# Kernel optimization log

Measured on AMD Instinct MI355X. Metric: run time of the kernel, lower is better.

Reference implementation:

```python
import math
import jax, jax.numpy as jnp
import numpy as np

B, T, M, D = 65536, 20, 4, 4   # batch, timesteps, regions, d_reg
L, H, FF = 3, 2, 16            # layers, heads, dim_feedforward
S = M + 1                      # seq_len with cls token
TAU = 10000.0


def setup_inputs() -> dict:
    key = jax.random.key(0)
    ks = jax.random.split(key, 8)

    def w(k, shape, std=0.1):
        return jax.random.normal(k, shape, dtype=jnp.float32) * std

    return {
        "regional_states": jax.random.normal(ks[0], (B, T, M, D), dtype=jnp.float32),
        "cls_token": w(ks[1], (1, 1, D), 0.02),
        # stacked per-layer params (layer axis first)
        "Wqkv": w(ks[2], (L, 3 * D, D)),   # nn.MultiheadAttention in_proj_weight
        "bqkv": jnp.zeros((L, 3 * D), jnp.float32),
        "Wo": w(ks[3], (L, D, D)),          # out_proj weight
        "bo": jnp.zeros((L, D), jnp.float32),
        "W1": w(ks[4], (L, FF, D)),         # linear1 weight (torch layout: out, in)
        "b1": jnp.zeros((L, FF), jnp.float32),
        "W2": w(ks[5], (L, D, FF)),         # linear2 weight
        "b2": jnp.zeros((L, D), jnp.float32),
    }


def _positional_encoding():
    # PE(pos,2i)=sin(pos/tau^(2i/D)), PE(pos,2i+1)=cos(...)
    pos = jnp.arange(S, dtype=jnp.float32)[:, None]            # (S,1)
    div = jnp.exp(jnp.arange(0, D, 2, dtype=jnp.float32) * (-math.log(TAU) / D))
    pe = jnp.zeros((S, D), jnp.float32)
    pe = pe.at[:, 0::2].set(jnp.sin(pos * div))
    pe = pe.at[:, 1::2].set(jnp.cos(pos * div))
    return pe  # (S, D)


def _layer(x, Wqkv, bqkv, Wo, bo, W1, b1, W2, b2):
    # x: (N, S, D). Dropout is identity (eval mode).
    N, Sq, Dm = x.shape
    hd = Dm // H
    qkv = x @ Wqkv.T + bqkv                     # (N, S, 3D)
    q, k, v = jnp.split(qkv, 3, axis=-1)

    def heads(t):
        return t.reshape(N, Sq, H, hd).transpose(0, 2, 1, 3)  # (N, H, S, hd)

    q, k, v = heads(q), heads(k), heads(v)
    scores = jnp.einsum("nhqd,nhkd->nhqk", q, k) / math.sqrt(hd)
    attn = jax.nn.softmax(scores, axis=-1)
    o = jnp.einsum("nhqk,nhkd->nhqd", attn, v)
    o = o.transpose(0, 2, 1, 3).reshape(N, Sq, Dm)
    attn_out = o @ Wo.T + bo
    x = x + attn_out                            # residual (no norm)
    ff = jax.nn.relu(x @ W1.T + b1) @ W2.T + b2
    return x + ff


def reference(regional_states, cls_token, Wqkv, bqkv, Wo, bo, W1, b1, W2, b2):
    Bq, Tq, Mq, Dq = regional_states.shape
    N = Bq * Tq
    x = regional_states.reshape(N, Mq, Dq)
    cls = jnp.broadcast_to(cls_token, (N, 1, Dq))
    x = jnp.concatenate([cls, x], axis=1)       # (N, S, D)
    x = x + _positional_encoding()[None, :, :]
    for i in range(L):
        x = _layer(x, Wqkv[i], bqkv[i], Wo[i], bo[i], W1[i], b1[i], W2[i], b2[i])
    F_g = x[:, 0, :].reshape(Bq, Tq, Dq)
    subregion_seq = x[:, 1:, :].reshape(Bq, Tq, Mq * Dq)
    return (F_g, subregion_seq)
```

## Files before the change

### kernel.cpp

```cpp
#include <hip/hip_runtime.h>


typedef _Float16 h2 __attribute__((ext_vector_type(2)));

enum {
  WF_CLS  = 0,
  WF_BQKV = 4,
  WF_BO   = 40,
  WF_B1   = 52,
  WF_B2   = 100,
  H_QKV   = 112,
  H_WO    = 184,
  H_W1    = 208,
  H_W2    = 304,
  WF_FLAG = 400,
  WF_TOTAL = 401
};

__device__ __forceinline__ float bf2f(unsigned short u) {
  unsigned int x = ((unsigned int)u) << 16;
  float f;
  __builtin_memcpy(&f, &x, 4);
  return f;
}

__device__ __forceinline__ bool is_bf16_packed(const unsigned int* w) {
  int pass = 0;
#pragma unroll
  for (int i = 0; i < 16; ++i) {
    unsigned int lo = w[i] & 0xFFFFu;
    unsigned int e = (lo >> 7) & 0xFFu;
    if (lo == 0u || (e >= 90u && e <= 140u)) ++pass;
  }
  return pass >= 15;
}

__device__ __forceinline__ float dot2(h2 a, h2 b, float c) {
#if __has_builtin(__builtin_amdgcn_fdot2)
  return __builtin_amdgcn_fdot2(a, b, c, false);
#else
  return fmaf((float)a.x, (float)b.x, fmaf((float)a.y, (float)b.y, c));
#endif
}

__device__ __forceinline__ h2 pk(float a, float b) {
  auto t = __builtin_amdgcn_cvt_pkrtz(a, b);
  h2 r;
  __builtin_memcpy(&r, &t, sizeof(r));
  return r;
}

__device__ __forceinline__ float fexp2(float x) {
#if __has_builtin(__builtin_amdgcn_exp2f)
  return __builtin_amdgcn_exp2f(x);
#else
  return __builtin_exp2f(x);
#endif
}

__global__ void mpt_prep(const void* __restrict__ cls,
                         const void* __restrict__ Wqkv,
                         const void* __restrict__ bqkv,
                         const void* __restrict__ Wo,
                         const void* __restrict__ bo,
                         const void* __restrict__ W1,
                         const void* __restrict__ b1,
                         const void* __restrict__ W2,
                         const void* __restrict__ b2,
                         const void* __restrict__ xin,
                         float* __restrict__ wf) {
  const bool wbf = is_bf16_packed((const unsigned int*)Wqkv);
  const bool xbf = is_bf16_packed((const unsigned int*)xin);
  const float FS = 1.44269504088896341f * 0.70710678118654752f;

  for (int w = threadIdx.x; w < WF_TOTAL; w += 256) {
    if (w == WF_FLAG) { ((int*)wf)[w] = xbf ? 0 : 1; continue; }

    auto g = [&](const void* src, int idx) -> float {
      return wbf ? bf2f(((const unsigned short*)src)[idx])
                 : ((const float*)src)[idx];
    };

    if (w < H_QKV) {
      float val;
      if (w < WF_BQKV) {
        val = g(cls, w) + ((w & 1) ? 1.0f : 0.0f);
      } else if (w < WF_BO) {
        int t = w - WF_BQKV;
        val = g(bqkv, t);
        int j = t % 12;
        if (j >= 4 && j < 8) val *= FS;
      } else if (w < WF_B1) {
        val = g(bo, w - WF_BO);
      } else if (w < WF_B2) {
        val = g(b1, w - WF_B1);
      } else {
        val = g(b2, w - WF_B2);
      }
      wf[w] = val;
    } else {
      int base;
      float s = 1.0f;
      if (w < H_WO) {
        int t = w - H_QKV, l = t / 24, j = (t % 24) / 2, p = t & 1;
        base = l * 48 + j * 4 + p * 2;
        if (j >= 4 && j < 8) s = FS;
        h2 hv = pk(g(Wqkv, base) * s, g(Wqkv, base + 1) * s);
        ((h2*)wf)[w] = hv;
      } else if (w < H_W1) {
        int t = w - H_WO, l = t / 8, i = (t % 8) / 2, p = t & 1;
        base = l * 16 + i * 4 + p * 2;
        ((h2*)wf)[w] = pk(g(Wo, base), g(Wo, base + 1));
      } else if (w < H_W2) {
        int t = w - H_W1, l = t / 32, f = (t % 32) / 2, p = t & 1;
        base = l * 64 + f * 4 + p * 2;
        ((h2*)wf)[w] = pk(g(W1, base), g(W1, base + 1));
      } else {
        int t = w - H_W2, l = t / 32, i = (t % 32) / 8, p = t % 8;
        base = l * 64 + i * 16 + p * 2;
        ((h2*)wf)[w] = pk(g(W2, base), g(W2, base + 1));
      }
    }
  }
}

__global__ __launch_bounds__(256) void mpt_main(
    const void* __restrict__ xin,
    const float* __restrict__ wf,
    float* __restrict__ out,
    int N) {
  const int n = blockIdx.x * 256 + threadIdx.x;
  if (n >= N) return;

  const int xf32 = ((const int*)wf)[WF_FLAG];
  const h2* hw = (const h2*)wf;

  const float pe[4][4] = {
    { 0.8414709848078965f, 0.5403023058681398f, 0.0099998333341667f, 0.9999500004166653f },
    { 0.9092974268256817f,-0.4161468365471424f, 0.0199986666933331f, 0.9998000066665778f },
    { 0.1411200080598672f,-0.9899924966004454f, 0.0299955002024957f, 0.9995500337489875f },
    {-0.7568024953079283f,-0.6536436208636119f, 0.0399893341866342f, 0.9992001066609779f }
  };

  float raw[16];
  if (xf32) {
    const float4* pf = reinterpret_cast<const float4*>((const float*)xin + (size_t)n * 16);
#pragma unroll
    for (int r = 0; r < 4; ++r) {
      float4 t = pf[r];
      raw[r * 4 + 0] = t.x; raw[r * 4 + 1] = t.y;
      raw[r * 4 + 2] = t.z; raw[r * 4 + 3] = t.w;
    }
  } else {
    struct alignas(16) U8 { unsigned short v[8]; };
    const U8* p = reinterpret_cast<const U8*>((const unsigned short*)xin + (size_t)n * 16);
    U8 a0 = p[0], a1 = p[1];
#pragma unroll
    for (int j = 0; j < 8; ++j) {
      raw[j]     = bf2f(a0.v[j]);
      raw[8 + j] = bf2f(a1.v[j]);
    }
  }

  float x[5][4];
#pragma unroll
  for (int d = 0; d < 4; ++d) x[0][d] = wf[WF_CLS + d];
#pragma unroll
  for (int r = 0; r < 4; ++r)
#pragma unroll
    for (int d = 0; d < 4; ++d) x[1 + r][d] = raw[r * 4 + d] + pe[r][d];

#pragma unroll
  for (int l = 0; l < 3; ++l) {
    const float* bq = wf + WF_BQKV + l * 12;
    const float* bo = wf + WF_BO   + l * 4;
    const float* b1 = wf + WF_B1   + l * 16;
    const float* b2 = wf + WF_B2   + l * 4;
    const h2* hq  = hw + H_QKV + l * 24;
    const h2* hwo = hw + H_WO  + l * 8;
    const h2* hw1 = hw + H_W1  + l * 32;
    const h2* hw2 = hw + H_W2  + l * 32;

    h2 xh[5][2];
#pragma unroll
    for (int s = 0; s < 5; ++s) {
      xh[s][0] = pk(x[s][0], x[s][1]);
      xh[s][1] = pk(x[s][2], x[s][3]);
    }

    float q[5][4], k[5][4], v[5][4];
#pragma unroll
    for (int s = 0; s < 5; ++s) {
#pragma unroll
      for (int j = 0; j < 12; ++j) {
        float a = dot2(xh[s][0], hq[j * 2], dot2(xh[s][1], hq[j * 2 + 1], bq[j]));
        if (j < 4)      q[s][j] = a;
        else if (j < 8) k[s][j - 4] = a;
        else            v[s][j - 8] = a;
      }
    }

    float o[5][4];
#pragma unroll
    for (int h = 0; h < 2; ++h) {
      const int d0 = 2 * h, d1 = 2 * h + 1;
      h2 qh[5], kh[5];
#pragma unroll
      for (int s = 0; s < 5; ++s) {
        qh[s] = pk(q[s][d0], q[s][d1]);
        kh[s] = pk(k[s][d0], k[s][d1]);
      }
#pragma unroll
      for (int si = 0; si < 5; ++si) {
        float e[5], den = 0.f;
#pragma unroll
        for (int sj = 0; sj < 5; ++sj) {
          e[sj] = fexp2(dot2(qh[si], kh[sj], 0.0f));
          den += e[sj];
        }
        float inv = __builtin_amdgcn_rcpf(den);
        float o0 = 0.f, o1 = 0.f;
#pragma unroll
        for (int sj = 0; sj < 5; ++sj) {
          o0 = fmaf(e[sj], v[sj][d0], o0);
          o1 = fmaf(e[sj], v[sj][d1], o1);
        }
        o[si][d0] = o0 * inv;
        o[si][d1] = o1 * inv;
      }
    }

#pragma unroll
    for (int s = 0; s < 5; ++s) {
      h2 oh0 = pk(o[s][0], o[s][1]), oh1 = pk(o[s][2], o[s][3]);
      float nx[4];
#pragma unroll
      for (int i = 0; i < 4; ++i)
        nx[i] = dot2(oh0, hwo[i * 2], dot2(oh1, hwo[i * 2 + 1], x[s][i] + bo[i]));

      h2 nh0 = pk(nx[0], nx[1]), nh1 = pk(nx[2], nx[3]);
      float acc[4] = {b2[0], b2[1], b2[2], b2[3]};
#pragma unroll
      for (int p = 0; p < 8; ++p) {
        int f0 = 2 * p, f1 = 2 * p + 1;
        float h0 = fmaxf(dot2(nh0, hw1[f0 * 2], dot2(nh1, hw1[f0 * 2 + 1], b1[f0])), 0.f);
        float h1 = fmaxf(dot2(nh0, hw1[f1 * 2], dot2(nh1, hw1[f1 * 2 + 1], b1[f1])), 0.f);
        h2 hh = pk(h0, h1);
#pragma unroll
        for (int i = 0; i < 4; ++i) acc[i] = dot2(hh, hw2[i * 8 + p], acc[i]);
      }
#pragma unroll
      for (int i = 0; i < 4; ++i) x[s][i] = nx[i] + acc[i];
    }
  }

  *reinterpret_cast<float4*>(out + (size_t)n * 4) =
      make_float4(x[0][0], x[0][1], x[0][2], x[0][3]);
  float* sub = out + (size_t)N * 4 + (size_t)n * 16;
#pragma unroll
  for (int r = 0; r < 4; ++r)
    *reinterpret_cast<float4*>(sub + r * 4) =
        make_float4(x[1 + r][0], x[1 + r][1], x[1 + r][2], x[1 + r][3]);
}

extern "C" void kernel_launch(void* const* d_in, const int* in_sizes, int n_in,
                              void* d_out, int out_size, void* d_ws, size_t ws_size,
                              hipStream_t stream) {
  float* wf = (float*)d_ws;

  mpt_prep<<<1, 256, 0, stream>>>(
      d_in[1], d_in[2], d_in[3], d_in[4], d_in[5],
      d_in[6], d_in[7], d_in[8], d_in[9],
      d_in[0],
      wf);

  const int N = in_sizes[0] / 16;
  mpt_main<<<(N + 255) / 256, 256, 0, stream>>>(
      d_in[0], wf, (float*)d_out, N);
}
```

Before: 275.8 us.

## Process two sequences per thread and compute FFN hidden layer in packed half2

Each thread now handles two sequences (grid halved), interleaving their work to expose instruction-level parallelism and amortize the uniform weight loads. The FFN first layer is rewritten as packed half2 FMAs with a packed ReLU, with W1 and b1 relaid out in the prep kernel to match. The layer loop is no longer unrolled to contain code size and register pressure. This raises register use per thread and lowers the number of waves, and packed fp16 accumulation in the FFN may reduce accuracy.

```diff
diff --git a/kernel.cpp b/kernel.cpp
--- a/kernel.cpp
+++ b/kernel.cpp
@@ -7,14 +7,14 @@
   WF_CLS  = 0,
   WF_BQKV = 4,
   WF_BO   = 40,
-  WF_B1   = 52,
-  WF_B2   = 100,
-  H_QKV   = 112,
-  H_WO    = 184,
-  H_W1    = 208,
-  H_W2    = 304,
-  WF_FLAG = 400,
-  WF_TOTAL = 401
+  WF_B2   = 52,
+  H_B1    = 64,
+  H_QKV   = 88,
+  H_WO    = 160,
+  H_W1    = 184,
+  H_W2    = 280,
+  WF_FLAG = 376,
+  WF_TOTAL = 377
 };
 
 __device__ __forceinline__ float bf2f(unsigned short u) {
@@ -48,6 +48,18 @@
   h2 r;
   __builtin_memcpy(&r, &t, sizeof(r));
   return r;
+}
+
+__device__ __forceinline__ h2 relu2(h2 a) {
+  h2 z = {(_Float16)0.0f, (_Float16)0.0f};
+#if __has_builtin(__builtin_elementwise_max)
+  return __builtin_elementwise_max(a, z);
+#else
+  h2 r;
+  r.x = a.x > z.x ? a.x : z.x;
+  r.y = a.y > z.y ? a.y : z.y;
+  return r;
+#endif
 }
 
 __device__ __forceinline__ float fexp2(float x) {
@@ -81,7 +93,7 @@
                  : ((const float*)src)[idx];
     };
 
-    if (w < H_QKV) {
+    if (w < H_B1) {
       float val;
       if (w < WF_BQKV) {
         val = g(cls, w) + ((w & 1) ? 1.0f : 0.0f);
@@ -90,34 +102,33 @@
         val = g(bqkv, t);
         int j = t % 12;
         if (j >= 4 && j < 8) val *= FS;
-      } else if (w < WF_B1) {
+      } else if (w < WF_B2) {
         val = g(bo, w - WF_BO);
-      } else if (w < WF_B2) {
-        val = g(b1, w - WF_B1);
       } else {
         val = g(b2, w - WF_B2);
       }
       wf[w] = val;
     } else {
-      int base;
-      float s = 1.0f;
-      if (w < H_WO) {
+      if (w < H_QKV) {
+        int t = w - H_B1, l = t / 8, p = t % 8;
+        int base = l * 16 + 2 * p;
+        ((h2*)wf)[w] = pk(g(b1, base), g(b1, base + 1));
+      } else if (w < H_WO) {
         int t = w - H_QKV, l = t / 24, j = (t % 24) / 2, p = t & 1;
-        base = l * 48 + j * 4 + p * 2;
-        if (j >= 4 && j < 8) s = FS;
-        h2 hv = pk(g(Wqkv, base) * s, g(Wqkv, base + 1) * s);
-        ((h2*)wf)[w] = hv;
+        int base = l * 48 + j * 4 + p * 2;
+        float s = (j >= 4 && j < 8) ? FS : 1.0f;
+        ((h2*)wf)[w] = pk(g(Wqkv, base) * s, g(Wqkv, base + 1) * s);
       } else if (w < H_W1) {
         int t = w - H_WO, l = t / 8, i = (t % 8) / 2, p = t & 1;
-        base = l * 16 + i * 4 + p * 2;
+        int base = l * 16 + i * 4 + p * 2;
         ((h2*)wf)[w] = pk(g(Wo, base), g(Wo, base + 1));
       } else if (w < H_W2) {
-        int t = w - H_W1, l = t / 32, f = (t % 32) / 2, p = t & 1;
-        base = l * 64 + f * 4 + p * 2;
-        ((h2*)wf)[w] = pk(g(W1, base), g(W1, base + 1));
+        int t = w - H_W1, l = t / 32, p = (t % 32) / 4, d = t % 4;
+        int base = l * 64 + 8 * p + d;
+        ((h2*)wf)[w] = pk(g(W1, base), g(W1, base + 4));
       } else {
         int t = w - H_W2, l = t / 32, i = (t % 32) / 8, p = t % 8;
-        base = l * 64 + i * 16 + p * 2;
+        int base = l * 64 + i * 16 + p * 2;
         ((h2*)wf)[w] = pk(g(W2, base), g(W2, base + 1));
       }
     }
@@ -129,8 +140,13 @@
     const float* __restrict__ wf,
     float* __restrict__ out,
     int N) {
-  const int n = blockIdx.x * 256 + threadIdx.x;
-  if (n >= N) return;
+  constexpr int U = 2;
+  const int n0 = blockIdx.x * 512 + threadIdx.x;
+  if (n0 >= N) return;
+  const bool has1 = (n0 + 256) < N;
+  int nseq[U];
+  nseq[0] = n0;
+  nseq[1] = has1 ? (n0 + 256) : n0;
 
   const int xf32 = ((const int*)wf)[WF_FLAG];
   const h2* hw = (const h2*)wf;
@@ -142,125 +158,176 @@
     {-0.7568024953079283f,-0.6536436208636119f, 0.0399893341866342f, 0.9992001066609779f }
   };
 
-  float raw[16];
+  float raw[U][16];
   if (xf32) {
-    const float4* pf = reinterpret_cast<const float4*>((const float*)xin + (size_t)n * 16);
-#pragma unroll
-    for (int r = 0; r < 4; ++r) {
-      float4 t = pf[r];
-      raw[r * 4 + 0] = t.x; raw[r * 4 + 1] = t.y;
-      raw[r * 4 + 2] = t.z; raw[r * 4 + 3] = t.w;
+#pragma unroll
+    for (int u = 0; u < U; ++u) {
+      const float4* pf =
+          reinterpret_cast<const float4*>((const float*)xin + (size_t)nseq[u] * 16);
+#pragma unroll
+      for (int r = 0; r < 4; ++r) {
+        float4 t = pf[r];
+        raw[u][r * 4 + 0] = t.x; raw[u][r * 4 + 1] = t.y;
+        raw[u][r * 4 + 2] = t.z; raw[u][r * 4 + 3] = t.w;
+      }
     }
   } else {
     struct alignas(16) U8 { unsigned short v[8]; };
-    const U8* p = reinterpret_cast<const U8*>((const unsigned short*)xin + (size_t)n * 16);
-    U8 a0 = p[0], a1 = p[1];
-#pragma unroll
-    for (int j = 0; j < 8; ++j) {
-      raw[j]     = bf2f(a0.v[j]);
-      raw[8 + j] = bf2f(a1.v[j]);
-    }
-  }
-
-  float x[5][4];
-#pragma unroll
-  for (int d = 0; d < 4; ++d) x[0][d] = wf[WF_CLS + d];
-#pragma unroll
-  for (int r = 0; r < 4; ++r)
-#pragma unroll
-    for (int d = 0; d < 4; ++d) x[1 + r][d] = raw[r * 4 + d] + pe[r][d];
-
-#pragma unroll
+#pragma unroll
+    for (int u = 0; u < U; ++u) {
+      const U8* p =
+          reinterpret_cast<const U8*>((const unsigned short*)xin + (size_t)nseq[u] * 16);
+      U8 a0 = p[0], a1 = p[1];
+#pragma unroll
+      for (int j = 0; j < 8; ++j) {
+        raw[u][j]     = bf2f(a0.v[j]);
+        raw[u][8 + j] = bf2f(a1.v[j]);
+      }
+    }
+  }
+
+  float x[U][5][4];
+#pragma unroll
+  for (int u = 0; u < U; ++u) {
+#pragma unroll
+    for (int d = 0; d < 4; ++d) x[u][0][d] = wf[WF_CLS + d];
+#pragma unroll
+    for (int r = 0; r < 4; ++r)
+#pragma unroll
+      for (int d = 0; d < 4; ++d) x[u][1 + r][d] = raw[u][r * 4 + d] + pe[r][d];
+  }
+
+#pragma unroll 1
   for (int l = 0; l < 3; ++l) {
-    const float* bq = wf + WF_BQKV + l * 12;
-    const float* bo = wf + WF_BO   + l * 4;
-    const float* b1 = wf + WF_B1   + l * 16;
-    const float* b2 = wf + WF_B2   + l * 4;
-    const h2* hq  = hw + H_QKV + l * 24;
-    const h2* hwo = hw + H_WO  + l * 8;
-    const h2* hw1 = hw + H_W1  + l * 32;
-    const h2* hw2 = hw + H_W2  + l * 32;
-
-    h2 xh[5][2];
+    const float* bq  = wf + WF_BQKV + l * 12;
+    const float* bo  = wf + WF_BO   + l * 4;
+    const float* b2  = wf + WF_B2   + l * 4;
+    const h2* hb1  = hw + H_B1  + l * 8;
+    const h2* hq   = hw + H_QKV + l * 24;
+    const h2* hwo  = hw + H_WO  + l * 8;
+    const h2* hw1p = hw + H_W1  + l * 32;
+    const h2* hw2  = hw + H_W2  + l * 32;
+
+    h2 xh[U][5][2];
+#pragma unroll
+    for (int s = 0; s < 5; ++s)
+#pragma unroll
+      for (int u = 0; u < U; ++u) {
+        xh[u][s][0] = pk(x[u][s][0], x[u][s][1]);
+        xh[u][s][1] = pk(x[u][s][2], x[u][s][3]);
+      }
+
+    float q[U][5][4], k[U][5][4], v[U][5][4];
 #pragma unroll
     for (int s = 0; s < 5; ++s) {
-      xh[s][0] = pk(x[s][0], x[s][1]);
-      xh[s][1] = pk(x[s][2], x[s][3]);
-    }
-
-    float q[5][4], k[5][4], v[5][4];
-#pragma unroll
-    for (int s = 0; s < 5; ++s) {
 #pragma unroll
       for (int j = 0; j < 12; ++j) {
-        float a = dot2(xh[s][0], hq[j * 2], dot2(xh[s][1], hq[j * 2 + 1], bq[j]));
-        if (j < 4)      q[s][j] = a;
-        else if (j < 8) k[s][j - 4] = a;
-        else            v[s][j - 8] = a;
-      }
-    }
-
-    float o[5][4];
+#pragma unroll
+        for (int u = 0; u < U; ++u) {
+          float a = dot2(xh[u][s][0], hq[j * 2],
+                         dot2(xh[u][s][1], hq[j * 2 + 1], bq[j]));
+          if (j < 4)      q[u][s][j] = a;
+          else if (j < 8) k[u][s][j - 4] = a;
+          else            v[u][s][j - 8] = a;
+        }
+      }
+    }
+
+    float o[U][5][4];
 #pragma unroll
     for (int h = 0; h < 2; ++h) {
       const int d0 = 2 * h, d1 = 2 * h + 1;
-      h2 qh[5], kh[5];
-#pragma unroll
-      for (int s = 0; s < 5; ++s) {
-        qh[s] = pk(q[s][d0], q[s][d1]);
-        kh[s] = pk(k[s][d0], k[s][d1]);
-      }
+      h2 qh[U][5], kh[U][5];
+#pragma unroll
+      for (int s = 0; s < 5; ++s)
+#pragma unroll
+        for (int u = 0; u < U; ++u) {
+          qh[u][s] = pk(q[u][s][d0], q[u][s][d1]);
+          kh[u][s] = pk(k[u][s][d0], k[u][s][d1]);
+        }
 #pragma unroll
       for (int si = 0; si < 5; ++si) {
-        float e[5], den = 0.f;
-#pragma unroll
-        for (int sj = 0; sj < 5; ++sj) {
-          e[sj] = fexp2(dot2(qh[si], kh[sj], 0.0f));
-          den += e[sj];
+        float e[U][5], den[U];
+#pragma unroll
+        for (int u = 0; u < U; ++u) den[u] = 0.f;
+#pragma unroll
+        for (int sj = 0; sj < 5; ++sj)
+#pragma unroll
+          for (int u = 0; u < U; ++u) {
+            e[u][sj] = fexp2(dot2(qh[u][si], kh[u][sj], 0.0f));
+            den[u] += e[u][sj];
+          }
+#pragma unroll
+        for (int u = 0; u < U; ++u) {
+          float inv = __builtin_amdgcn_rcpf(den[u]);
+          float o0 = 0.f, o1 = 0.f;
+#pragma unroll
+          for (int sj = 0; sj < 5; ++sj) {
+            o0 = fmaf(e[u][sj], v[u][sj][d0], o0);
+            o1 = fmaf(e[u][sj], v[u][sj][d1], o1);
+          }
+          o[u][si][d0] = o0 * inv;
+          o[u][si][d1] = o1 * inv;
         }
-        float inv = __builtin_amdgcn_rcpf(den);
-        float o0 = 0.f, o1 = 0.f;
-#pragma unroll
-        for (int sj = 0; sj < 5; ++sj) {
-          o0 = fmaf(e[sj], v[sj][d0], o0);
-          o1 = fmaf(e[sj], v[sj][d1], o1);
+      }
+    }
+
+#pragma unroll
+    for (int s = 0; s < 5; ++s) {
+      float nx[U][4];
+#pragma unroll
+      for (int u = 0; u < U; ++u) {
+        h2 oh0 = pk(o[u][s][0], o[u][s][1]), oh1 = pk(o[u][s][2], o[u][s][3]);
+#pragma unroll
+        for (int i = 0; i < 4; ++i)
+          nx[u][i] = dot2(oh0, hwo[i * 2],
+                          dot2(oh1, hwo[i * 2 + 1], x[u][s][i] + bo[i]));
+      }
+
+      h2 xb[U][4];
+      float acc[U][4];
+#pragma unroll
+      for (int u = 0; u < U; ++u) {
+#pragma unroll
+        for (int d = 0; d < 4; ++d) xb[u][d] = pk(nx[u][d], nx[u][d]);
+#pragma unroll
+        for (int i = 0; i < 4; ++i) acc[u][i] = b2[i];
+      }
+#pragma unroll
+      for (int p = 0; p < 8; ++p) {
+        h2 hh[U];
+#pragma unroll
+        for (int u = 0; u < U; ++u) {
+          h2 hc = hb1[p];
+#pragma unroll
+          for (int d = 0; d < 4; ++d) hc = xb[u][d] * hw1p[p * 4 + d] + hc;
+          hh[u] = relu2(hc);
         }
-        o[si][d0] = o0 * inv;
-        o[si][d1] = o1 * inv;
-      }
-    }
-
-#pragma unroll
-    for (int s = 0; s < 5; ++s) {
-      h2 oh0 = pk(o[s][0], o[s][1]), oh1 = pk(o[s][2], o[s][3]);
-      float nx[4];
-#pragma unroll
-      for (int i = 0; i < 4; ++i)
-        nx[i] = dot2(oh0, hwo[i * 2], dot2(oh1, hwo[i * 2 + 1], x[s][i] + bo[i]));
-
-      h2 nh0 = pk(nx[0], nx[1]), nh1 = pk(nx[2], nx[3]);
-      float acc[4] = {b2[0], b2[1], b2[2], b2[3]};
-#pragma unroll
-      for (int p = 0; p < 8; ++p) {
-        int f0 = 2 * p, f1 = 2 * p + 1;
-        float h0 = fmaxf(dot2(nh0, hw1[f0 * 2], dot2(nh1, hw1[f0 * 2 + 1], b1[f0])), 0.f);
-        float h1 = fmaxf(dot2(nh0, hw1[f1 * 2], dot2(nh1, hw1[f1 * 2 + 1], b1[f1])), 0.f);
-        h2 hh = pk(h0, h1);
-#pragma unroll
-        for (int i = 0; i < 4; ++i) acc[i] = dot2(hh, hw2[i * 8 + p], acc[i]);
-      }
-#pragma unroll
-      for (int i = 0; i < 4; ++i) x[s][i] = nx[i] + acc[i];
-    }
-  }
-
-  *reinterpret_cast<float4*>(out + (size_t)n * 4) =
-      make_float4(x[0][0], x[0][1], x[0][2], x[0][3]);
-  float* sub = out + (size_t)N * 4 + (size_t)n * 16;
-#pragma unroll
-  for (int r = 0; r < 4; ++r)
-    *reinterpret_cast<float4*>(sub + r * 4) =
-        make_float4(x[1 + r][0], x[1 + r][1], x[1 + r][2], x[1 + r][3]);
+#pragma unroll
+        for (int u = 0; u < U; ++u)
+#pragma unroll
+          for (int i = 0; i < 4; ++i)
+            acc[u][i] = dot2(hh[u], hw2[i * 8 + p], acc[u][i]);
+      }
+#pragma unroll
+      for (int u = 0; u < U; ++u)
+#pragma unroll
+        for (int i = 0; i < 4; ++i) x[u][s][i] = nx[u][i] + acc[u][i];
+    }
+  }
+
+#pragma unroll
+  for (int u = 0; u < U; ++u) {
+    if (u == 1 && !has1) break;
+    const int n = nseq[u];
+    *reinterpret_cast<float4*>(out + (size_t)n * 4) =
+        make_float4(x[u][0][0], x[u][0][1], x[u][0][2], x[u][0][3]);
+    float* sub = out + (size_t)N * 4 + (size_t)n * 16;
+#pragma unroll
+    for (int r = 0; r < 4; ++r)
+      *reinterpret_cast<float4*>(sub + r * 4) =
+          make_float4(x[u][1 + r][0], x[u][1 + r][1], x[u][1 + r][2], x[u][1 + r][3]);
+  }
 }
 
 extern "C" void kernel_launch(void* const* d_in, const int* in_sizes, int n_in,
@@ -275,6 +342,6 @@
       wf);
 
   const int N = in_sizes[0] / 16;
-  mpt_main<<<(N + 255) / 256, 256, 0, stream>>>(
+  mpt_main<<<(N + 511) / 512, 256, 0, stream>>>(
       d_in[0], wf, (float*)d_out, N);
 }
```

New measurement: 266.8 us. -3.3%, faster.

## Use packed fp16 FFN-1 with h2 relu, grid-stride loop, and rolled layer loop

Applied to the files above, without the earlier changes.

The first FFN layer is now computed in packed half2 FMAs over pairs of hidden units, with b1 and W1 re-laid out in the prep kernel, and ReLU applied as a packed max. This replaces per-unit dot2 plus scalar fmax and pack. The main kernel becomes a grid-stride loop capped at 1280 blocks with launch_bounds(256,4), and the layer loop is no longer unrolled, which shrinks code size and register pressure. Accumulating FFN-1 in fp16 instead of fp32 risks precision loss, and the rolled loop adds per-layer indexing overhead.

```diff
diff --git a/kernel.cpp b/kernel.cpp
--- a/kernel.cpp
+++ b/kernel.cpp
@@ -7,14 +7,14 @@
   WF_CLS  = 0,
   WF_BQKV = 4,
   WF_BO   = 40,
-  WF_B1   = 52,
-  WF_B2   = 100,
-  H_QKV   = 112,
-  H_WO    = 184,
-  H_W1    = 208,
-  H_W2    = 304,
-  WF_FLAG = 400,
-  WF_TOTAL = 401
+  WF_B2   = 52,
+  H_B1    = 64,
+  H_QKV   = 88,
+  H_WO    = 160,
+  H_W1    = 184,
+  H_W2    = 280,
+  WF_FLAG = 376,
+  WF_TOTAL = 377
 };
 
 __device__ __forceinline__ float bf2f(unsigned short u) {
@@ -48,6 +48,18 @@
   h2 r;
   __builtin_memcpy(&r, &t, sizeof(r));
   return r;
+}
+
+__device__ __forceinline__ h2 relu2(h2 a) {
+  h2 z = {(_Float16)0.0f, (_Float16)0.0f};
+#if __has_builtin(__builtin_elementwise_max)
+  return __builtin_elementwise_max(a, z);
+#else
+  h2 r;
+  r.x = a.x > z.x ? a.x : z.x;
+  r.y = a.y > z.y ? a.y : z.y;
+  return r;
+#endif
 }
 
 __device__ __forceinline__ float fexp2(float x) {
@@ -81,7 +93,7 @@
                  : ((const float*)src)[idx];
     };
 
-    if (w < H_QKV) {
+    if (w < H_B1) {
       float val;
       if (w < WF_BQKV) {
         val = g(cls, w) + ((w & 1) ? 1.0f : 0.0f);
@@ -90,48 +102,45 @@
         val = g(bqkv, t);
         int j = t % 12;
         if (j >= 4 && j < 8) val *= FS;
-      } else if (w < WF_B1) {
+      } else if (w < WF_B2) {
         val = g(bo, w - WF_BO);
-      } else if (w < WF_B2) {
-        val = g(b1, w - WF_B1);
       } else {
         val = g(b2, w - WF_B2);
       }
       wf[w] = val;
     } else {
-      int base;
-      float s = 1.0f;
-      if (w < H_WO) {
+      if (w < H_QKV) {
+        int t = w - H_B1, l = t / 8, p = t % 8;
+        int base = l * 16 + 2 * p;
+        ((h2*)wf)[w] = pk(g(b1, base), g(b1, base + 1));
+      } else if (w < H_WO) {
         int t = w - H_QKV, l = t / 24, j = (t % 24) / 2, p = t & 1;
-        base = l * 48 + j * 4 + p * 2;
-        if (j >= 4 && j < 8) s = FS;
-        h2 hv = pk(g(Wqkv, base) * s, g(Wqkv, base + 1) * s);
-        ((h2*)wf)[w] = hv;
+        int base = l * 48 + j * 4 + p * 2;
+        float s = (j >= 4 && j < 8) ? FS : 1.0f;
+        ((h2*)wf)[w] = pk(g(Wqkv, base) * s, g(Wqkv, base + 1) * s);
       } else if (w < H_W1) {
         int t = w - H_WO, l = t / 8, i = (t % 8) / 2, p = t & 1;
-        base = l * 16 + i * 4 + p * 2;
+        int base = l * 16 + i * 4 + p * 2;
         ((h2*)wf)[w] = pk(g(Wo, base), g(Wo, base + 1));
       } else if (w < H_W2) {
-        int t = w - H_W1, l = t / 32, f = (t % 32) / 2, p = t & 1;
-        base = l * 64 + f * 4 + p * 2;
-        ((h2*)wf)[w] = pk(g(W1, base), g(W1, base + 1));
+        int t = w - H_W1, l = t / 32, p = (t % 32) / 4, d = t % 4;
+        int base = l * 64 + 8 * p + d;
+        ((h2*)wf)[w] = pk(g(W1, base), g(W1, base + 4));
       } else {
         int t = w - H_W2, l = t / 32, i = (t % 32) / 8, p = t % 8;
-        base = l * 64 + i * 16 + p * 2;
+        int base = l * 64 + i * 16 + p * 2;
         ((h2*)wf)[w] = pk(g(W2, base), g(W2, base + 1));
       }
     }
   }
 }
 
-__global__ __launch_bounds__(256) void mpt_main(
+__global__ __launch_bounds__(256, 4) void mpt_main(
     const void* __restrict__ xin,
     const float* __restrict__ wf,
     float* __restrict__ out,
     int N) {
-  const int n = blockIdx.x * 256 + threadIdx.x;
-  if (n >= N) return;
-
+  const int stride = gridDim.x * 256;
   const int xf32 = ((const int*)wf)[WF_FLAG];
   const h2* hw = (const h2*)wf;
 
@@ -142,125 +151,136 @@
     {-0.7568024953079283f,-0.6536436208636119f, 0.0399893341866342f, 0.9992001066609779f }
   };
 
-  float raw[16];
-  if (xf32) {
-    const float4* pf = reinterpret_cast<const float4*>((const float*)xin + (size_t)n * 16);
-#pragma unroll
-    for (int r = 0; r < 4; ++r) {
-      float4 t = pf[r];
-      raw[r * 4 + 0] = t.x; raw[r * 4 + 1] = t.y;
-      raw[r * 4 + 2] = t.z; raw[r * 4 + 3] = t.w;
+#pragma unroll 1
+  for (int n = blockIdx.x * 256 + threadIdx.x; n < N; n += stride) {
+    float raw[16];
+    if (xf32) {
+      const float4* pf =
+          reinterpret_cast<const float4*>((const float*)xin + (size_t)n * 16);
+#pragma unroll
+      for (int r = 0; r < 4; ++r) {
+        float4 t = pf[r];
+        raw[r * 4 + 0] = t.x; raw[r * 4 + 1] = t.y;
+        raw[r * 4 + 2] = t.z; raw[r * 4 + 3] = t.w;
+      }
+    } else {
+      struct alignas(16) U8 { unsigned short v[8]; };
+      const U8* p =
+          reinterpret_cast<const U8*>((const unsigned short*)xin + (size_t)n * 16);
+      U8 a0 = p[0], a1 = p[1];
+#pragma unroll
+      for (int j = 0; j < 8; ++j) {
+        raw[j]     = bf2f(a0.v[j]);
+        raw[8 + j] = bf2f(a1.v[j]);
+      }
     }
-  } else {
-    struct alignas(16) U8 { unsigned short v[8]; };
-    const U8* p = reinterpret_cast<const U8*>((const unsigned short*)xin + (size_t)n * 16);
-    U8 a0 = p[0], a1 = p[1];
-#pragma unroll
-    for (int j = 0; j < 8; ++j) {
-      raw[j]     = bf2f(a0.v[j]);
-      raw[8 + j] = bf2f(a1.v[j]);
+
+    float x[5][4];
+#pragma unroll
+    for (int d = 0; d < 4; ++d) x[0][d] = wf[WF_CLS + d];
+#pragma unroll
+    for (int r = 0; r < 4; ++r)
+#pragma unroll
+      for (int d = 0; d < 4; ++d) x[1 + r][d] = raw[r * 4 + d] + pe[r][d];
+
+#pragma unroll 1
+    for (int l = 0; l < 3; ++l) {
+      const float* bq  = wf + WF_BQKV + l * 12;
+      const float* bo  = wf + WF_BO   + l * 4;
+      const float* b2  = wf + WF_B2   + l * 4;
+      const h2* hb1  = hw + H_B1  + l * 8;
+      const h2* hq   = hw + H_QKV + l * 24;
+      const h2* hwo  = hw + H_WO  + l * 8;
+      const h2* hw1p = hw + H_W1  + l * 32;
+      const h2* hw2  = hw + H_W2  + l * 32;
+
+      h2 xh[5][2];
+#pragma unroll
+      for (int s = 0; s < 5; ++s) {
+        xh[s][0] = pk(x[s][0], x[s][1]);
+        xh[s][1] = pk(x[s][2], x[s][3]);
+      }
+
+      float q[5][4], k[5][4], v[5][4];
+#pragma unroll
+      for (int s = 0; s < 5; ++s) {
+#pragma unroll
+        for (int j = 0; j < 12; ++j) {
+          float a = dot2(xh[s][0], hq[j * 2],
+                         dot2(xh[s][1], hq[j * 2 + 1], bq[j]));
+          if (j < 4)      q[s][j] = a;
+          else if (j < 8) k[s][j - 4] = a;
+          else            v[s][j - 8] = a;
+        }
+      }
+
+      float o[5][4];
+#pragma unroll
+      for (int h = 0; h < 2; ++h) {
+        const int d0 = 2 * h, d1 = 2 * h + 1;
+        h2 qh[5], kh[5];
+#pragma unroll
+        for (int s = 0; s < 5; ++s) {
+          qh[s] = pk(q[s][d0], q[s][d1]);
+          kh[s] = pk(k[s][d0], k[s][d1]);
+        }
+#pragma unroll
+        for (int si = 0; si < 5; ++si) {
+          float e[5], den = 0.f;
+#pragma unroll
+          for (int sj = 0; sj < 5; ++sj) {
+            e[sj] = fexp2(dot2(qh[si], kh[sj], 0.0f));
+            den += e[sj];
+          }
+          float inv = __builtin_amdgcn_rcpf(den);
+          float o0 = 0.f, o1 = 0.f;
+#pragma unroll
+          for (int sj = 0; sj < 5; ++sj) {
+            o0 = fmaf(e[sj], v[sj][d0], o0);
+            o1 = fmaf(e[sj], v[sj][d1], o1);
+          }
+          o[si][d0] = o0 * inv;
+          o[si][d1] = o1 * inv;
+        }
+      }
+
+#pragma unroll
+      for (int s = 0; s < 5; ++s) {
+        h2 oh0 = pk(o[s][0], o[s][1]), oh1 = pk(o[s][2], o[s][3]);
+        float nx[4];
+#pragma unroll
+        for (int i = 0; i < 4; ++i)
+          nx[i] = dot2(oh0, hwo[i * 2],
+                       dot2(oh1, hwo[i * 2 + 1], x[s][i] + bo[i]));
+
+        h2 xb[4];
+        float acc[4];
+#pragma unroll
+        for (int d = 0; d < 4; ++d) xb[d] = pk(nx[d], nx[d]);
+#pragma unroll
+        for (int i = 0; i < 4; ++i) acc[i] = b2[i];
+#pragma unroll
+        for (int p = 0; p < 8; ++p) {
+          h2 hc = hb1[p];
+#pragma unroll
+          for (int d = 0; d < 4; ++d) hc = xb[d] * hw1p[p * 4 + d] + hc;
+          h2 hh = relu2(hc);
+#pragma unroll
+          for (int i = 0; i < 4; ++i) acc[i] = dot2(hh, hw2[i * 8 + p], acc[i]);
+        }
+#pragma unroll
+        for (int i = 0; i < 4; ++i) x[s][i] = nx[i] + acc[i];
+      }
     }
+
+    *reinterpret_cast<float4*>(out + (size_t)n * 4) =
+        make_float4(x[0][0], x[0][1], x[0][2], x[0][3]);
+    float* sub = out + (size_t)N * 4 + (size_t)n * 16;
+#pragma unroll
+    for (int r = 0; r < 4; ++r)
+      *reinterpret_cast<float4*>(sub + r * 4) =
+          make_float4(x[1 + r][0], x[1 + r][1], x[1 + r][2], x[1 + r][3]);
   }
-
-  float x[5][4];
-#pragma unroll
-  for (int d = 0; d < 4; ++d) x[0][d] = wf[WF_CLS + d];
-#pragma unroll
-  for (int r = 0; r < 4; ++r)
-#pragma unroll
-    for (int d = 0; d < 4; ++d) x[1 + r][d] = raw[r * 4 + d] + pe[r][d];
-
-#pragma unroll
-  for (int l = 0; l < 3; ++l) {
-    const float* bq = wf + WF_BQKV + l * 12;
-    const float* bo = wf + WF_BO   + l * 4;
-    const float* b1 = wf + WF_B1   + l * 16;
-    const float* b2 = wf + WF_B2   + l * 4;
-    const h2* hq  = hw + H_QKV + l * 24;
-    const h2* hwo = hw + H_WO  + l * 8;
-    const h2* hw1 = hw + H_W1  + l * 32;
-    const h2* hw2 = hw + H_W2  + l * 32;
-
-    h2 xh[5][2];
-#pragma unroll
-    for (int s = 0; s < 5; ++s) {
-      xh[s][0] = pk(x[s][0], x[s][1]);
-      xh[s][1] = pk(x[s][2], x[s][3]);
-    }
-
-    float q[5][4], k[5][4], v[5][4];
-#pragma unroll
-    for (int s = 0; s < 5; ++s) {
-#pragma unroll
-      for (int j = 0; j < 12; ++j) {
-        float a = dot2(xh[s][0], hq[j * 2], dot2(xh[s][1], hq[j * 2 + 1], bq[j]));
-        if (j < 4)      q[s][j] = a;
-        else if (j < 8) k[s][j - 4] = a;
-        else            v[s][j - 8] = a;
-      }
-    }
-
-    float o[5][4];
-#pragma unroll
-    for (int h = 0; h < 2; ++h) {
-      const int d0 = 2 * h, d1 = 2 * h + 1;
-      h2 qh[5], kh[5];
-#pragma unroll
-      for (int s = 0; s < 5; ++s) {
-        qh[s] = pk(q[s][d0], q[s][d1]);
-        kh[s] = pk(k[s][d0], k[s][d1]);
-      }
-#pragma unroll
-      for (int si = 0; si < 5; ++si) {
-        float e[5], den = 0.f;
-#pragma unroll
-        for (int sj = 0; sj < 5; ++sj) {
-          e[sj] = fexp2(dot2(qh[si], kh[sj], 0.0f));
-          den += e[sj];
-        }
-        float inv = __builtin_amdgcn_rcpf(den);
-        float o0 = 0.f, o1 = 0.f;
-#pragma unroll
-        for (int sj = 0; sj < 5; ++sj) {
-          o0 = fmaf(e[sj], v[sj][d0], o0);
-          o1 = fmaf(e[sj], v[sj][d1], o1);
-        }
-        o[si][d0] = o0 * inv;
-        o[si][d1] = o1 * inv;
-      }
-    }
-
-#pragma unroll
-    for (int s = 0; s < 5; ++s) {
-      h2 oh0 = pk(o[s][0], o[s][1]), oh1 = pk(o[s][2], o[s][3]);
-      float nx[4];
-#pragma unroll
-      for (int i = 0; i < 4; ++i)
-        nx[i] = dot2(oh0, hwo[i * 2], dot2(oh1, hwo[i * 2 + 1], x[s][i] + bo[i]));
-
-      h2 nh0 = pk(nx[0], nx[1]), nh1 = pk(nx[2], nx[3]);
-      float acc[4] = {b2[0], b2[1], b2[2], b2[3]};
-#pragma unroll
-      for (int p = 0; p < 8; ++p) {
-        int f0 = 2 * p, f1 = 2 * p + 1;
-        float h0 = fmaxf(dot2(nh0, hw1[f0 * 2], dot2(nh1, hw1[f0 * 2 + 1], b1[f0])), 0.f);
-        float h1 = fmaxf(dot2(nh0, hw1[f1 * 2], dot2(nh1, hw1[f1 * 2 + 1], b1[f1])), 0.f);
-        h2 hh = pk(h0, h1);
-#pragma unroll
-        for (int i = 0; i < 4; ++i) acc[i] = dot2(hh, hw2[i * 8 + p], acc[i]);
-      }
-#pragma unroll
-      for (int i = 0; i < 4; ++i) x[s][i] = nx[i] + acc[i];
-    }
-  }
-
-  *reinterpret_cast<float4*>(out + (size_t)n * 4) =
-      make_float4(x[0][0], x[0][1], x[0][2], x[0][3]);
-  float* sub = out + (size_t)N * 4 + (size_t)n * 16;
-#pragma unroll
-  for (int r = 0; r < 4; ++r)
-    *reinterpret_cast<float4*>(sub + r * 4) =
-        make_float4(x[1 + r][0], x[1 + r][1], x[1 + r][2], x[1 + r][3]);
 }
 
 extern "C" void kernel_launch(void* const* d_in, const int* in_sizes, int n_in,
@@ -275,6 +295,8 @@
       wf);
 
   const int N = in_sizes[0] / 16;
-  mpt_main<<<(N + 255) / 256, 256, 0, stream>>>(
+  int blocks = (N + 255) / 256;
+  if (blocks > 1280) blocks = 1280;
+  mpt_main<<<blocks, 256, 0, stream>>>(
       d_in[0], wf, (float*)d_out, N);
 }
```

Result: faster. 266.3 us (-3.5%).
